# Kernel optimization log

Hardware: AMD Instinct MI355X
Metric: run time of the kernel (lower is better)

The kernel has to match this reference:

```python
import jax, jax.numpy as jnp
import numpy as np

B, S, E, H = 2, 2048, 1024, 16
D = E // H  # head_dim = 64

def setup_inputs() -> dict:
    key = jax.random.key(0)
    ks = jax.random.split(key, 9)
    scale = 1.0 / np.sqrt(E)
    inp = {"x": jax.random.normal(ks[0], (B, S, E), dtype=jnp.float32)}
    for i, name in enumerate(["q", "k", "v", "o"]):
        inp[f"W{name}"] = jax.random.uniform(ks[1 + 2 * i], (E, E), jnp.float32, -scale, scale)
        inp[f"b{name}"] = jax.random.uniform(ks[2 + 2 * i], (E,), jnp.float32, -scale, scale)
    return inp

def reference(x, Wq, bq, Wk, bk, Wv, bv, Wo, bo):
    b, s, e = x.shape
    q = x @ Wq + bq
    k = x @ Wk + bk
    v = x @ Wv + bv
    # Faithful to source: view(B, H, S, D) with NO transpose -> splits the
    # sequence dimension across heads (each head sees a contiguous chunk of
    # s*d elements reinterpreted as [s, d]).
    q = q.reshape(b, H, s, D)
    k = k.reshape(b, H, s, D)
    v = v.reshape(b, H, s, D)
    scores = jnp.einsum("bhqd,bhkd->bhqk", q, k) / np.sqrt(D)
    # mask=False in source still adds a zeros mask (no-op); omitted.
    probs = jax.nn.softmax(scores, axis=-1)
    xhat = jnp.einsum("bhqk,bhkd->bhqd", probs, v)
    # transpose(1, 2).contiguous().view(B, S, E)
    xhat = xhat.transpose(0, 2, 1, 3).reshape(b, s, e)
    return xhat @ Wo + bo
```

## Files before the change

kernel.cpp:

```cpp
#include <hip/hip_runtime.h>
#include <hip/hip_bf16.h>
#include <math.h>

#define B_ 2
#define S_ 2048
#define E_ 1024
#define H_ 16
#define D_ 64

typedef __attribute__((ext_vector_type(8))) short short8;
typedef __attribute__((ext_vector_type(4))) float f32x4;
typedef __attribute__((ext_vector_type(4))) unsigned short us4;
typedef __attribute__((ext_vector_type(8))) unsigned short us8;
typedef unsigned short ushort_t;

#define MFMA16 __builtin_amdgcn_mfma_f32_16x16x32_bf16

__device__ __forceinline__ ushort_t f2bf(float f) {
    unsigned int u = __float_as_uint(f);
    u += 0x7FFFu + ((u >> 16) & 1u);
    return (ushort_t)(u >> 16);
}
__device__ __forceinline__ float bf2f(ushort_t h) {
    return __uint_as_float((unsigned int)h << 16);
}
__device__ __forceinline__ ushort_t f2bf_fast(float f) {
    __hip_bfloat16 h = __float2bfloat16(f);
    return *reinterpret_cast<ushort_t*>(&h);
}

__device__ __forceinline__ void gload16(const void* g, void* l) {
    __builtin_amdgcn_global_load_lds(
        (__attribute__((address_space(1))) void*)(unsigned long long)g,
        (__attribute__((address_space(3))) void*)(unsigned int)(unsigned long long)l,
        16, 0, 0);
}

__global__ __launch_bounds__(256)
void split_x(const float* __restrict__ in, ushort_t* __restrict__ hi)
{
    const size_t base = ((size_t)blockIdx.x * 256 + threadIdx.x) * 8;
    float v[8];
    *reinterpret_cast<float4*>(&v[0]) = *reinterpret_cast<const float4*>(&in[base]);
    *reinterpret_cast<float4*>(&v[4]) = *reinterpret_cast<const float4*>(&in[base + 4]);
    us8 h;
#pragma unroll
    for (int j = 0; j < 8; ++j) h[j] = f2bf(v[j]);
    *reinterpret_cast<us8*>(&hi[base]) = h;
}

__global__ __launch_bounds__(256)
void wsplit_t(const float* __restrict__ Wq, const float* __restrict__ Wk,
              const float* __restrict__ Wv, const float* __restrict__ Wo,
              ushort_t* __restrict__ Wth, ushort_t* __restrict__ Wtl)
{
    __shared__ float T[64][65];
    const int tid = threadIdx.x;
    const int z = blockIdx.z;
    const float* W = (z == 0) ? Wq : (z == 1) ? Wk : (z == 2) ? Wv : Wo;
    const int kt = blockIdx.y * 64;
    const int nt = blockIdx.x * 64;

    const int lr = (tid >> 4) * 4;
    const int lc = (tid & 15) * 4;
#pragma unroll
    for (int i = 0; i < 4; ++i) {
        float4 v = *reinterpret_cast<const float4*>(&W[(size_t)(kt + lr + i) * 1024 + nt + lc]);
        T[lr + i][lc + 0] = v.x; T[lr + i][lc + 1] = v.y;
        T[lr + i][lc + 2] = v.z; T[lr + i][lc + 3] = v.w;
    }
    __syncthreads();

    const int n = tid >> 2;
    const int kc = (tid & 3) * 16;
    us8 h[2], l[2];
#pragma unroll
    for (int u = 0; u < 2; ++u)
#pragma unroll
        for (int j = 0; j < 8; ++j) {
            float v = T[kc + u * 8 + j][n];
            ushort_t hh = f2bf(v);
            h[u][j] = hh;
            l[u][j] = f2bf(v - bf2f(hh));
        }
    ushort_t* dh = Wth + ((size_t)z * 1024 + nt + n) * 1024 + kt + kc;
    ushort_t* dl = Wtl + ((size_t)z * 1024 + nt + n) * 1024 + kt + kc;
    *reinterpret_cast<us8*>(dh)     = h[0];
    *reinterpret_cast<us8*>(dh + 8) = h[1];
    *reinterpret_cast<us8*>(dl)     = l[0];
    *reinterpret_cast<us8*>(dl + 8) = l[1];
}

__global__ __launch_bounds__(256, 3)
void gemm_qkv(const ushort_t* __restrict__ xh, const ushort_t* __restrict__ Wth,
              const float* __restrict__ bq, const float* __restrict__ bk,
              const float* __restrict__ bv,
              ushort_t* __restrict__ Qb, ushort_t* __restrict__ Kb,
              ushort_t* __restrict__ Vb, float qalpha)
{
    __shared__ ushort_t As[128 * 32], Bs[128 * 32];
    const int which = blockIdx.x >> 3;
    const int n0 = (blockIdx.x & 7) * 128;
    const int m0 = blockIdx.y * 128;
    const ushort_t* Bh = Wth + (size_t)which * 1024 * 1024;
    const float* bias = (which == 0) ? bq : (which == 1) ? bk : bv;
    ushort_t* out = (which == 0) ? Qb : (which == 1) ? Kb : Vb;
    const float alpha = (which == 0) ? qalpha : 1.0f;

    const int tid  = threadIdx.x;
    const int lane = tid & 63;
    const int w    = tid >> 6;
    const int l15  = lane & 15;
    const int g    = lane >> 4;
    const int wr   = w >> 1;
    const int wc   = w & 1;

    const int sr  = lane >> 2;
    const int scz = (lane & 3) ^ ((sr >> 1) & 3);
    const int sc  = scz * 8;
    const int j0 = w * 2, j1 = j0 + 1;

    const ushort_t* gA0 = xh + (size_t)(m0 + j0 * 16 + sr) * 1024 + sc;
    const ushort_t* gA1 = xh + (size_t)(m0 + j1 * 16 + sr) * 1024 + sc;
    const ushort_t* gB0 = Bh + (size_t)(n0 + j0 * 16 + sr) * 1024 + sc;
    const ushort_t* gB1 = Bh + (size_t)(n0 + j1 * 16 + sr) * 1024 + sc;

    const int sx  = (l15 >> 1) & 3;
    const int rd1 = (((g >> 1) + 0) ^ sx) * 8 + (g & 1) * 4;
    const int rd2 = (((g >> 1) + 2) ^ sx) * 8 + (g & 1) * 4;

    f32x4 acc[4][4];
#pragma unroll
    for (int i = 0; i < 4; ++i)
#pragma unroll
        for (int j = 0; j < 4; ++j) { acc[i][j][0] = 0.f; acc[i][j][1] = 0.f; acc[i][j][2] = 0.f; acc[i][j][3] = 0.f; }

    for (int kt = 0; kt < 32; ++kt) {
        const int k0 = kt * 32;
        if (kt) __syncthreads();
        gload16(gA0 + k0, As + j0 * 512);
        gload16(gA1 + k0, As + j1 * 512);
        gload16(gB0 + k0, Bs + j0 * 512);
        gload16(gB1 + k0, Bs + j1 * 512);
        asm volatile("s_waitcnt vmcnt(0)" ::: "memory");
        __syncthreads();

        short8 bh[4];
#pragma unroll
        for (int nb = 0; nb < 4; ++nb) {
            const int rb = (wc * 64 + nb * 16 + l15) * 32;
            union { us4 h[2]; short8 s; } u;
            u.h[0] = *reinterpret_cast<const us4*>(Bs + rb + rd1);
            u.h[1] = *reinterpret_cast<const us4*>(Bs + rb + rd2);
            bh[nb] = u.s;
        }
#pragma unroll
        for (int mb = 0; mb < 4; ++mb) {
            const int rb = (wr * 64 + mb * 16 + l15) * 32;
            union { us4 h[2]; short8 s; } ua;
            ua.h[0] = *reinterpret_cast<const us4*>(As + rb + rd1);
            ua.h[1] = *reinterpret_cast<const us4*>(As + rb + rd2);
            const short8 ah = ua.s;
#pragma unroll
            for (int nb = 0; nb < 4; ++nb)
                acc[mb][nb] = MFMA16(ah, bh[nb], acc[mb][nb], 0, 0, 0);
        }
    }

    float bvv[4];
#pragma unroll
    for (int nb = 0; nb < 4; ++nb) bvv[nb] = bias[n0 + wc * 64 + nb * 16 + l15];
#pragma unroll
    for (int mb = 0; mb < 4; ++mb)
#pragma unroll
        for (int r = 0; r < 4; ++r) {
            const size_t row = m0 + wr * 64 + mb * 16 + 4 * g + r;
#pragma unroll
            for (int nb = 0; nb < 4; ++nb) {
                const float vv = (acc[mb][nb][r] + bvv[nb]) * alpha;
                out[row * 1024 + n0 + wc * 64 + nb * 16 + l15] = f2bf(vv);
            }
        }
}

__global__ __launch_bounds__(256, 2)
void gemm_o64(const ushort_t* __restrict__ Ah, const ushort_t* __restrict__ Al,
              const ushort_t* __restrict__ Bh, const ushort_t* __restrict__ Bl,
              const float* __restrict__ bias, float* __restrict__ out)
{
    __shared__ ushort_t AsH[128 * 32], AsL[128 * 32], BsH[64 * 32], BsL[64 * 32];
    const int tid  = threadIdx.x;
    const int lane = tid & 63;
    const int w    = tid >> 6;
    const int l15  = lane & 15;
    const int g    = lane >> 4;
    const int wr   = w >> 1;
    const int wc   = w & 1;
    const int n0 = blockIdx.x * 64;
    const int m0 = blockIdx.y * 128;

    const int sr  = lane >> 2;
    const int scz = (lane & 3) ^ ((sr >> 1) & 3);
    const int sc  = scz * 8;
    const int ja0 = 2 * w, ja1 = 2 * w + 1;

    const ushort_t* gAh0 = Ah + (size_t)(m0 + ja0 * 16 + sr) * 1024 + sc;
    const ushort_t* gAh1 = Ah + (size_t)(m0 + ja1 * 16 + sr) * 1024 + sc;
    const ushort_t* gAl0 = Al + (size_t)(m0 + ja0 * 16 + sr) * 1024 + sc;
    const ushort_t* gAl1 = Al + (size_t)(m0 + ja1 * 16 + sr) * 1024 + sc;
    const ushort_t* gBh0 = Bh + (size_t)(n0 + w * 16 + sr) * 1024 + sc;
    const ushort_t* gBl0 = Bl + (size_t)(n0 + w * 16 + sr) * 1024 + sc;

    const int sx  = (l15 >> 1) & 3;
    const int rd1 = (((g >> 1) + 0) ^ sx) * 8 + (g & 1) * 4;
    const int rd2 = (((g >> 1) + 2) ^ sx) * 8 + (g & 1) * 4;

    f32x4 acc[4][2];
#pragma unroll
    for (int i = 0; i < 4; ++i)
#pragma unroll
        for (int j = 0; j < 2; ++j) { acc[i][j][0] = 0.f; acc[i][j][1] = 0.f; acc[i][j][2] = 0.f; acc[i][j][3] = 0.f; }

    for (int kt = 0; kt < 32; ++kt) {
        const int k0 = kt * 32;
        if (kt) __syncthreads();
        gload16(gAh0 + k0, AsH + ja0 * 512);
        gload16(gAh1 + k0, AsH + ja1 * 512);
        gload16(gAl0 + k0, AsL + ja0 * 512);
        gload16(gAl1 + k0, AsL + ja1 * 512);
        gload16(gBh0 + k0, BsH + w * 512);
        gload16(gBl0 + k0, BsL + w * 512);
        asm volatile("s_waitcnt vmcnt(0)" ::: "memory");
        __syncthreads();

        short8 bh[2], bl[2];
#pragma unroll
        for (int nb = 0; nb < 2; ++nb) {
            const int rb = (wc * 32 + nb * 16 + l15) * 32;
            union { us4 h[2]; short8 s; } u;
            u.h[0] = *reinterpret_cast<const us4*>(BsH + rb + rd1);
            u.h[1] = *reinterpret_cast<const us4*>(BsH + rb + rd2);
            bh[nb] = u.s;
            union { us4 h[2]; short8 s; } v;
            v.h[0] = *reinterpret_cast<const us4*>(BsL + rb + rd1);
            v.h[1] = *reinterpret_cast<const us4*>(BsL + rb + rd2);
            bl[nb] = v.s;
        }
#pragma unroll
        for (int mb = 0; mb < 4; ++mb) {
            const int rb = (wr * 64 + mb * 16 + l15) * 32;
            union { us4 h[2]; short8 s; } ua;
            ua.h[0] = *reinterpret_cast<const us4*>(AsH + rb + rd1);
            ua.h[1] = *reinterpret_cast<const us4*>(AsH + rb + rd2);
            union { us4 h[2]; short8 s; } ul;
            ul.h[0] = *reinterpret_cast<const us4*>(AsL + rb + rd1);
            ul.h[1] = *reinterpret_cast<const us4*>(AsL + rb + rd2);
            const short8 ah = ua.s, al = ul.s;
#pragma unroll
            for (int nb = 0; nb < 2; ++nb) {
                acc[mb][nb] = MFMA16(ah, bh[nb], acc[mb][nb], 0, 0, 0);
                acc[mb][nb] = MFMA16(al, bh[nb], acc[mb][nb], 0, 0, 0);
                acc[mb][nb] = MFMA16(ah, bl[nb], acc[mb][nb], 0, 0, 0);
            }
        }
    }

    float bvv[2];
#pragma unroll
    for (int nb = 0; nb < 2; ++nb) bvv[nb] = bias[n0 + wc * 32 + nb * 16 + l15];
#pragma unroll
    for (int mb = 0; mb < 4; ++mb)
#pragma unroll
        for (int r = 0; r < 4; ++r) {
            const size_t row = m0 + wr * 64 + mb * 16 + 4 * g + r;
#pragma unroll
            for (int nb = 0; nb < 2; ++nb)
                out[row * 1024 + n0 + wc * 32 + nb * 16 + l15] = acc[mb][nb][r] + bvv[nb];
        }
}

__global__ __launch_bounds__(256, 2)
void attn_mfma(const ushort_t* __restrict__ Q, const ushort_t* __restrict__ K,
               const ushort_t* __restrict__ V, ushort_t* __restrict__ XHh,
               ushort_t* __restrict__ XHl)
{
    __shared__ __align__(16) ushort_t Kf[4 * 2 * 64 * 8];
    __shared__ __align__(16) ushort_t Vf[4 * 2 * 64 * 8];

    const int tid  = threadIdx.x;
    const int w    = tid >> 6;
    const int lane = tid & 63;
    const int l15  = lane & 15;
    const int g    = lane >> 4;

    const int L  = blockIdx.x;
    const int qb = (L >> 3) & 15;
    const int bh = (L & 7) | ((L >> 7) << 3);
    const int b  = bh >> 4;
    const int hh = bh & 15;
    const size_t hoff = (size_t)b * S_ * E_ + (size_t)hh * S_ * D_;
    const ushort_t* Qh = Q + hoff;
    const ushort_t* Kh = K + hoff;
    const ushort_t* Vh = V + hoff;

    const int qw = qb * 128 + w * 32;

    short8 qf[2][2];
#pragma unroll
    for (int qg = 0; qg < 2; ++qg)
#pragma unroll
        for (int m = 0; m < 2; ++m) {
            const ushort_t* src = &Qh[(size_t)(qw + 16 * qg + l15) * D_ + 32 * m + 4 * g];
            us4 lo = *reinterpret_cast<const us4*>(src);
            us4 hi = *reinterpret_cast<const us4*>(src + 16);
            union { us4 h[2]; short8 s; } u;
            u.h[0] = lo; u.h[1] = hi;
            qf[qg][m] = u.s;
        }

    const int kr  = tid >> 2;
    const int kc0 = tid & 3;
    const int kkc = tid >> 4;
    const int vdc = tid & 15;
    const int vmc = kkc >> 3;
    const int vh  = (kkc >> 2) & 1;
    const int vg  = kkc & 3;
    const int vn  = vdc >> 2;

    f32x4 o[2][4];
#pragma unroll
    for (int qg = 0; qg < 2; ++qg)
#pragma unroll
        for (int n = 0; n < 4; ++n)
#pragma unroll
            for (int r = 0; r < 4; ++r) o[qg][n][r] = 0.f;

    float mrun[2] = {-1e30f, -1e30f};
    float lrun[2] = {0.f, 0.f};

    us8 kreg[2];
    us4 vreg[4];
#pragma unroll
    for (int u = 0; u < 2; ++u)
        kreg[u] = *reinterpret_cast<const us8*>(&Kh[(size_t)kr * D_ + 8 * (kc0 + 4 * u)]);
#pragma unroll
    for (int i = 0; i < 4; ++i)
        vreg[i] = *reinterpret_cast<const us4*>(&Vh[(size_t)(4 * kkc + i) * D_ + 4 * vdc]);

    for (int kt = 0; kt < S_ / 64; ++kt) {
        __syncthreads();

#pragma unroll
        for (int u = 0; u < 2; ++u) {
            const int c8 = kc0 + 4 * u;
            const int m = c8 >> 2;
            const int h = (c8 >> 1) & 1;
#pragma unroll
            for (int jh = 0; jh < 2; ++jh) {
                const int gk = (2 * c8 + jh) & 3;
                const int slot = gk * 16 + (kr & 15);
                us4 val;
#pragma unroll
                for (int i = 0; i < 4; ++i) val[i] = (ushort_t)kreg[u][4 * jh + i];
                *reinterpret_cast<us4*>(&Kf[((((kr >> 4) * 2 + m) * 64 + slot) * 8) + h * 4]) = val;
            }
        }
#pragma unroll
        for (int jj = 0; jj < 4; ++jj) {
            us4 val;
#pragma unroll
            for (int i = 0; i < 4; ++i) val[i] = vreg[i][jj];
            const int pos  = 4 * (vdc & 3) + jj;
            const int posx = pos ^ vg ^ (vn << 2);
            const int slot = vg * 16 + posx;
            *reinterpret_cast<us4*>(&Vf[(((vn * 2 + vmc) * 64 + slot) * 8) + vh * 4]) = val;
        }
        __syncthreads();

        if (kt + 1 < S_ / 64) {
            const int nt = kt + 1;
#pragma unroll
            for (int u = 0; u < 2; ++u)
                kreg[u] = *reinterpret_cast<const us8*>(&Kh[(size_t)(nt * 64 + kr) * D_ + 8 * (kc0 + 4 * u)]);
#pragma unroll
            for (int i = 0; i < 4; ++i)
                vreg[i] = *reinterpret_cast<const us4*>(&Vh[(size_t)(nt * 64 + 4 * kkc + i) * D_ + 4 * vdc]);
        }

        short8 kf[4][2];
#pragma unroll
        for (int kkb = 0; kkb < 4; ++kkb)
#pragma unroll
            for (int m = 0; m < 2; ++m)
                kf[kkb][m] = *reinterpret_cast<const short8*>(&Kf[((kkb * 2 + m) * 64 + lane) * 8]);

        f32x4 s[2][4];
#pragma unroll
        for (int qg = 0; qg < 2; ++qg)
#pragma unroll
            for (int kkb = 0; kkb < 4; ++kkb) {
                f32x4 z; z[0] = 0.f; z[1] = 0.f; z[2] = 0.f; z[3] = 0.f;
                z = MFMA16(kf[kkb][0], qf[qg][0], z, 0, 0, 0);
                s[qg][kkb] = MFMA16(kf[kkb][1], qf[qg][1], z, 0, 0, 0);
            }

        short8 vf[4][2];
#pragma unroll
        for (int n = 0; n < 4; ++n)
#pragma unroll
            for (int m = 0; m < 2; ++m) {
                const int posr = (lane & 15) ^ (lane >> 4) ^ (n << 2);
                const int slot = (lane & 48) | posr;
                vf[n][m] = *reinterpret_cast<const short8*>(&Vf[((n * 2 + m) * 64 + slot) * 8]);
            }

#pragma unroll
        for (int qg = 0; qg < 2; ++qg) {
            float t = s[qg][0][0];
#pragma unroll
            for (int kkb = 0; kkb < 4; ++kkb)
#pragma unroll
                for (int r = 0; r < 4; ++r) t = fmaxf(t, s[qg][kkb][r]);
            t = fmaxf(t, __shfl_xor(t, 16));
            t = fmaxf(t, __shfl_xor(t, 32));
            const float mnew = fmaxf(mrun[qg], t);
            const float corr = __builtin_amdgcn_exp2f(mrun[qg] - mnew);

            float rs = 0.f;
#pragma unroll
            for (int kkb = 0; kkb < 4; ++kkb)
#pragma unroll
                for (int r = 0; r < 4; ++r) {
                    const float p = __builtin_amdgcn_exp2f(s[qg][kkb][r] - mnew);
                    s[qg][kkb][r] = p;
                    rs += p;
                }
            rs += __shfl_xor(rs, 16);
            rs += __shfl_xor(rs, 32);
            lrun[qg] = lrun[qg] * corr + rs;
            mrun[qg] = mnew;

#pragma unroll
            for (int r = 0; r < 4; ++r) {
                const float c4 = __shfl(corr, 4 * g + r);
#pragma unroll
                for (int n = 0; n < 4; ++n) o[qg][n][r] *= c4;
            }

            short8 pa[2];
#pragma unroll
            for (int m = 0; m < 2; ++m) {
                us8 tmp;
#pragma unroll
                for (int r = 0; r < 4; ++r) {
                    tmp[r]     = f2bf_fast(s[qg][2 * m][r]);
                    tmp[r + 4] = f2bf_fast(s[qg][2 * m + 1][r]);
                }
                union { us8 u8; short8 s8; } cvt; cvt.u8 = tmp;
                pa[m] = cvt.s8;
            }
#pragma unroll
            for (int n = 0; n < 4; ++n) {
                o[qg][n] = MFMA16(pa[0], vf[n][0], o[qg][n], 0, 0, 0);
                o[qg][n] = MFMA16(pa[1], vf[n][1], o[qg][n], 0, 0, 0);
            }
        }
    }

#pragma unroll
    for (int qg = 0; qg < 2; ++qg) {
        const float invl = 1.f / lrun[qg];
#pragma unroll
        for (int r = 0; r < 4; ++r) {
            const float iv = __shfl(invl, 4 * g + r);
            const int row = qw + 16 * qg + 4 * g + r;
            const size_t base = ((size_t)b * S_ + row) * E_ + hh * D_ + l15;
#pragma unroll
            for (int n = 0; n < 4; ++n) {
                const float vv = o[qg][n][r] * iv;
                const ushort_t hi = f2bf(vv);
                XHh[base + 16 * n] = hi;
                XHl[base + 16 * n] = f2bf(vv - bf2f(hi));
            }
        }
    }
}

extern "C" void kernel_launch(void* const* d_in, const int* in_sizes, int n_in,
                              void* d_out, int out_size, void* d_ws, size_t ws_size,
                              hipStream_t stream) {
    (void)in_sizes; (void)n_in; (void)out_size; (void)ws_size;
    const float* x  = (const float*)d_in[0];
    const float* Wq = (const float*)d_in[1];
    const float* bq = (const float*)d_in[2];
    const float* Wk = (const float*)d_in[3];
    const float* bk = (const float*)d_in[4];
    const float* Wv = (const float*)d_in[5];
    const float* bv = (const float*)d_in[6];
    const float* Wo = (const float*)d_in[7];
    const float* bo = (const float*)d_in[8];
    float* out = (float*)d_out;

    char* ws = (char*)d_ws;
    const size_t MB8 = 8ull * 1024 * 1024;
    ushort_t* xhi = (ushort_t*)(ws);
    ushort_t* XHl = (ushort_t*)(ws + MB8);
    ushort_t* Wth = (ushort_t*)(ws + 2 * MB8);
    ushort_t* Wtl = (ushort_t*)(ws + 3 * MB8);
    ushort_t* Qb  = (ushort_t*)(ws + 4 * MB8);
    ushort_t* Kb  = (ushort_t*)(ws + 5 * MB8);
    ushort_t* Vb  = (ushort_t*)(ws + 6 * MB8);
    ushort_t* XHh = xhi;

    const float qalpha = 0.125f * 1.4426950408889634f;

    split_x<<<dim3(2048), dim3(256), 0, stream>>>(x, xhi);
    wsplit_t<<<dim3(16, 16, 4), dim3(256), 0, stream>>>(Wq, Wk, Wv, Wo, Wth, Wtl);

    gemm_qkv<<<dim3(24, 32), dim3(256), 0, stream>>>(xhi, Wth,
                                                     bq, bk, bv, Qb, Kb, Vb, qalpha);

    attn_mfma<<<dim3(512), dim3(256), 0, stream>>>(Qb, Kb, Vb, XHh, XHl);

    gemm_o64<<<dim3(16, 32), dim3(256), 0, stream>>>(XHh, XHl,
                                                     Wth + 3ull * 1024 * 1024,
                                                     Wtl + 3ull * 1024 * 1024,
                                                     bo, out);
}
```

Baseline: 159.5 us.

## Process 128-key tiles per iteration in attention, halving barriers and softmax rescales

The attention loop now handles 128 keys per iteration (two 64-key LDS halves) instead of 64. This halves the number of __syncthreads pairs and online-softmax max/corr/rescale steps per key. It drops the register prefetch of the next tile, so global loads are issued at the top of each iteration and waited on before the LDS stores. The larger score array also raises register pressure, which risks spills or lower occupancy under launch_bounds(256,2).

```diff
diff --git a/kernel.cpp b/kernel.cpp
--- a/kernel.cpp
+++ b/kernel.cpp
@@ -284,8 +284,8 @@
                const ushort_t* __restrict__ V, ushort_t* __restrict__ XHh,
                ushort_t* __restrict__ XHl)
 {
-    __shared__ __align__(16) ushort_t Kf[4 * 2 * 64 * 8];
-    __shared__ __align__(16) ushort_t Vf[4 * 2 * 64 * 8];
+    __shared__ __align__(16) ushort_t Kf[2][4 * 2 * 64 * 8];
+    __shared__ __align__(16) ushort_t Vf[2][4 * 2 * 64 * 8];
 
     const int tid  = threadIdx.x;
     const int w    = tid >> 6;
@@ -338,89 +338,78 @@
     float mrun[2] = {-1e30f, -1e30f};
     float lrun[2] = {0.f, 0.f};
 
-    us8 kreg[2];
-    us4 vreg[4];
-#pragma unroll
-    for (int u = 0; u < 2; ++u)
-        kreg[u] = *reinterpret_cast<const us8*>(&Kh[(size_t)kr * D_ + 8 * (kc0 + 4 * u)]);
-#pragma unroll
-    for (int i = 0; i < 4; ++i)
-        vreg[i] = *reinterpret_cast<const us4*>(&Vh[(size_t)(4 * kkc + i) * D_ + 4 * vdc]);
-
-    for (int kt = 0; kt < S_ / 64; ++kt) {
+    for (int kt = 0; kt < S_ / 128; ++kt) {
+        us8 kreg[2][2];
+        us4 vreg[2][4];
+#pragma unroll
+        for (int hf = 0; hf < 2; ++hf) {
+            const int rowb = kt * 128 + hf * 64;
+#pragma unroll
+            for (int u = 0; u < 2; ++u)
+                kreg[hf][u] = *reinterpret_cast<const us8*>(&Kh[(size_t)(rowb + kr) * D_ + 8 * (kc0 + 4 * u)]);
+#pragma unroll
+            for (int i = 0; i < 4; ++i)
+                vreg[hf][i] = *reinterpret_cast<const us4*>(&Vh[(size_t)(rowb + 4 * kkc + i) * D_ + 4 * vdc]);
+        }
+
         __syncthreads();
 
 #pragma unroll
-        for (int u = 0; u < 2; ++u) {
-            const int c8 = kc0 + 4 * u;
-            const int m = c8 >> 2;
-            const int h = (c8 >> 1) & 1;
-#pragma unroll
-            for (int jh = 0; jh < 2; ++jh) {
-                const int gk = (2 * c8 + jh) & 3;
-                const int slot = gk * 16 + (kr & 15);
+        for (int hf = 0; hf < 2; ++hf) {
+#pragma unroll
+            for (int u = 0; u < 2; ++u) {
+                const int c8 = kc0 + 4 * u;
+                const int m = c8 >> 2;
+                const int h = (c8 >> 1) & 1;
+#pragma unroll
+                for (int jh = 0; jh < 2; ++jh) {
+                    const int gk = (2 * c8 + jh) & 3;
+                    const int slot = gk * 16 + (kr & 15);
+                    us4 val;
+#pragma unroll
+                    for (int i = 0; i < 4; ++i) val[i] = (ushort_t)kreg[hf][u][4 * jh + i];
+                    *reinterpret_cast<us4*>(&Kf[hf][((((kr >> 4) * 2 + m) * 64 + slot) * 8) + h * 4]) = val;
+                }
+            }
+#pragma unroll
+            for (int jj = 0; jj < 4; ++jj) {
                 us4 val;
 #pragma unroll
-                for (int i = 0; i < 4; ++i) val[i] = (ushort_t)kreg[u][4 * jh + i];
-                *reinterpret_cast<us4*>(&Kf[((((kr >> 4) * 2 + m) * 64 + slot) * 8) + h * 4]) = val;
-            }
-        }
-#pragma unroll
-        for (int jj = 0; jj < 4; ++jj) {
-            us4 val;
-#pragma unroll
-            for (int i = 0; i < 4; ++i) val[i] = vreg[i][jj];
-            const int pos  = 4 * (vdc & 3) + jj;
-            const int posx = pos ^ vg ^ (vn << 2);
-            const int slot = vg * 16 + posx;
-            *reinterpret_cast<us4*>(&Vf[(((vn * 2 + vmc) * 64 + slot) * 8) + vh * 4]) = val;
+                for (int i = 0; i < 4; ++i) val[i] = vreg[hf][i][jj];
+                const int pos  = 4 * (vdc & 3) + jj;
+                const int posx = pos ^ vg ^ (vn << 2);
+                const int slot = vg * 16 + posx;
+                *reinterpret_cast<us4*>(&Vf[hf][(((vn * 2 + vmc) * 64 + slot) * 8) + vh * 4]) = val;
+            }
         }
         __syncthreads();
 
-        if (kt + 1 < S_ / 64) {
-            const int nt = kt + 1;
-#pragma unroll
-            for (int u = 0; u < 2; ++u)
-                kreg[u] = *reinterpret_cast<const us8*>(&Kh[(size_t)(nt * 64 + kr) * D_ + 8 * (kc0 + 4 * u)]);
-#pragma unroll
-            for (int i = 0; i < 4; ++i)
-                vreg[i] = *reinterpret_cast<const us4*>(&Vh[(size_t)(nt * 64 + 4 * kkc + i) * D_ + 4 * vdc]);
-        }
-
-        short8 kf[4][2];
-#pragma unroll
-        for (int kkb = 0; kkb < 4; ++kkb)
-#pragma unroll
-            for (int m = 0; m < 2; ++m)
-                kf[kkb][m] = *reinterpret_cast<const short8*>(&Kf[((kkb * 2 + m) * 64 + lane) * 8]);
-
-        f32x4 s[2][4];
-#pragma unroll
-        for (int qg = 0; qg < 2; ++qg)
-#pragma unroll
-            for (int kkb = 0; kkb < 4; ++kkb) {
-                f32x4 z; z[0] = 0.f; z[1] = 0.f; z[2] = 0.f; z[3] = 0.f;
-                z = MFMA16(kf[kkb][0], qf[qg][0], z, 0, 0, 0);
-                s[qg][kkb] = MFMA16(kf[kkb][1], qf[qg][1], z, 0, 0, 0);
-            }
-
-        short8 vf[4][2];
-#pragma unroll
-        for (int n = 0; n < 4; ++n)
-#pragma unroll
-            for (int m = 0; m < 2; ++m) {
-                const int posr = (lane & 15) ^ (lane >> 4) ^ (n << 2);
-                const int slot = (lane & 48) | posr;
-                vf[n][m] = *reinterpret_cast<const short8*>(&Vf[((n * 2 + m) * 64 + slot) * 8]);
-            }
+        f32x4 s[2][8];
+#pragma unroll
+        for (int hf = 0; hf < 2; ++hf) {
+            short8 kf[4][2];
+#pragma unroll
+            for (int kkb = 0; kkb < 4; ++kkb)
+#pragma unroll
+                for (int m = 0; m < 2; ++m)
+                    kf[kkb][m] = *reinterpret_cast<const short8*>(&Kf[hf][((kkb * 2 + m) * 64 + lane) * 8]);
+#pragma unroll
+            for (int qg = 0; qg < 2; ++qg)
+#pragma unroll
+                for (int kkb = 0; kkb < 4; ++kkb) {
+                    f32x4 z; z[0] = 0.f; z[1] = 0.f; z[2] = 0.f; z[3] = 0.f;
+                    z = MFMA16(kf[kkb][0], qf[qg][0], z, 0, 0, 0);
+                    s[qg][hf * 4 + kkb] = MFMA16(kf[kkb][1], qf[qg][1], z, 0, 0, 0);
+                }
+        }
 
 #pragma unroll
         for (int qg = 0; qg < 2; ++qg) {
             float t = s[qg][0][0];
 #pragma unroll
-            for (int kkb = 0; kkb < 4; ++kkb)
-#pragma unroll
-                for (int r = 0; r < 4; ++r) t = fmaxf(t, s[qg][kkb][r]);
+            for (int j = 0; j < 8; ++j)
+#pragma unroll
+                for (int r = 0; r < 4; ++r) t = fmaxf(t, s[qg][j][r]);
             t = fmaxf(t, __shfl_xor(t, 16));
             t = fmaxf(t, __shfl_xor(t, 32));
             const float mnew = fmaxf(mrun[qg], t);
@@ -428,11 +417,11 @@
 
             float rs = 0.f;
 #pragma unroll
-            for (int kkb = 0; kkb < 4; ++kkb)
+            for (int j = 0; j < 8; ++j)
 #pragma unroll
                 for (int r = 0; r < 4; ++r) {
-                    const float p = __builtin_amdgcn_exp2f(s[qg][kkb][r] - mnew);
-                    s[qg][kkb][r] = p;
+                    const float p = __builtin_amdgcn_exp2f(s[qg][j][r] - mnew);
+                    s[qg][j][r] = p;
                     rs += p;
                 }
             rs += __shfl_xor(rs, 16);
@@ -446,23 +435,38 @@
 #pragma unroll
                 for (int n = 0; n < 4; ++n) o[qg][n][r] *= c4;
             }
-
-            short8 pa[2];
-#pragma unroll
-            for (int m = 0; m < 2; ++m) {
-                us8 tmp;
-#pragma unroll
-                for (int r = 0; r < 4; ++r) {
-                    tmp[r]     = f2bf_fast(s[qg][2 * m][r]);
-                    tmp[r + 4] = f2bf_fast(s[qg][2 * m + 1][r]);
+        }
+
+#pragma unroll
+        for (int hf = 0; hf < 2; ++hf) {
+            short8 vf[4][2];
+#pragma unroll
+            for (int n = 0; n < 4; ++n)
+#pragma unroll
+                for (int m = 0; m < 2; ++m) {
+                    const int posr = (lane & 15) ^ (lane >> 4) ^ (n << 2);
+                    const int slot = (lane & 48) | posr;
+                    vf[n][m] = *reinterpret_cast<const short8*>(&Vf[hf][((n * 2 + m) * 64 + slot) * 8]);
                 }
-                union { us8 u8; short8 s8; } cvt; cvt.u8 = tmp;
-                pa[m] = cvt.s8;
-            }
-#pragma unroll
-            for (int n = 0; n < 4; ++n) {
-                o[qg][n] = MFMA16(pa[0], vf[n][0], o[qg][n], 0, 0, 0);
-                o[qg][n] = MFMA16(pa[1], vf[n][1], o[qg][n], 0, 0, 0);
+#pragma unroll
+            for (int qg = 0; qg < 2; ++qg) {
+                short8 pa[2];
+#pragma unroll
+                for (int m = 0; m < 2; ++m) {
+                    us8 tmp;
+#pragma unroll
+                    for (int r = 0; r < 4; ++r) {
+                        tmp[r]     = f2bf_fast(s[qg][hf * 4 + 2 * m][r]);
+                        tmp[r + 4] = f2bf_fast(s[qg][hf * 4 + 2 * m + 1][r]);
+                    }
+                    union { us8 u8; short8 s8; } cvt; cvt.u8 = tmp;
+                    pa[m] = cvt.s8;
+                }
+#pragma unroll
+                for (int n = 0; n < 4; ++n) {
+                    o[qg][n] = MFMA16(pa[0], vf[n][0], o[qg][n], 0, 0, 0);
+                    o[qg][n] = MFMA16(pa[1], vf[n][1], o[qg][n], 0, 0, 0);
+                }
             }
         }
     }
```

Result: faster. 150.7 us (-5.5%).

## Split attention KV range across two wave groups and merge softmax partials

Applied to the files above, without the earlier changes.

The attention kernel now launches 512 threads per block: two groups of four waves each handle half of the key/value sequence with separate shared-memory tiles. At the end, group 1 writes its partial outputs and running max/sum to LDS, and group 0 merges them flash-decoding style before storing. The aim is more parallelism and occupancy per query tile, trading away the register prefetch of the next K/V tile. It also adds an LDS merge step and tighter register limits from launch_bounds(512,4).

```diff
diff --git a/kernel.cpp b/kernel.cpp
--- a/kernel.cpp
+++ b/kernel.cpp
@@ -279,17 +279,20 @@
         }
 }
 
-__global__ __launch_bounds__(256, 2)
+__global__ __launch_bounds__(512, 4)
 void attn_mfma(const ushort_t* __restrict__ Q, const ushort_t* __restrict__ K,
                const ushort_t* __restrict__ V, ushort_t* __restrict__ XHh,
                ushort_t* __restrict__ XHl)
 {
-    __shared__ __align__(16) ushort_t Kf[4 * 2 * 64 * 8];
-    __shared__ __align__(16) ushort_t Vf[4 * 2 * 64 * 8];
+    __shared__ __align__(16) ushort_t SM[4][4096];
+    __shared__ float ML[4][2][16][2];
 
     const int tid  = threadIdx.x;
-    const int w    = tid >> 6;
+    const int w8   = tid >> 6;
+    const int grp  = w8 >> 2;
+    const int wl   = w8 & 3;
     const int lane = tid & 63;
+    const int ltid = tid & 255;
     const int l15  = lane & 15;
     const int g    = lane >> 4;
 
@@ -303,7 +306,7 @@
     const ushort_t* Kh = K + hoff;
     const ushort_t* Vh = V + hoff;
 
-    const int qw = qb * 128 + w * 32;
+    const int qw = qb * 128 + wl * 32;
 
     short8 qf[2][2];
 #pragma unroll
@@ -318,15 +321,18 @@
             qf[qg][m] = u.s;
         }
 
-    const int kr  = tid >> 2;
-    const int kc0 = tid & 3;
-    const int kkc = tid >> 4;
-    const int vdc = tid & 15;
+    const int kr  = ltid >> 2;
+    const int kc0 = ltid & 3;
+    const int kkc = ltid >> 4;
+    const int vdc = ltid & 15;
     const int vmc = kkc >> 3;
     const int vh  = (kkc >> 2) & 1;
     const int vg  = kkc & 3;
     const int vn  = vdc >> 2;
 
+    ushort_t* KfG = SM[grp];
+    ushort_t* VfG = SM[2 + grp];
+
     f32x4 o[2][4];
 #pragma unroll
     for (int qg = 0; qg < 2; ++qg)
@@ -338,16 +344,17 @@
     float mrun[2] = {-1e30f, -1e30f};
     float lrun[2] = {0.f, 0.f};
 
-    us8 kreg[2];
-    us4 vreg[4];
-#pragma unroll
-    for (int u = 0; u < 2; ++u)
-        kreg[u] = *reinterpret_cast<const us8*>(&Kh[(size_t)kr * D_ + 8 * (kc0 + 4 * u)]);
-#pragma unroll
-    for (int i = 0; i < 4; ++i)
-        vreg[i] = *reinterpret_cast<const us4*>(&Vh[(size_t)(4 * kkc + i) * D_ + 4 * vdc]);
-
-    for (int kt = 0; kt < S_ / 64; ++kt) {
+    for (int kt = 0; kt < 16; ++kt) {
+        const int rowb = grp * 1024 + kt * 64;
+        us8 kreg[2];
+#pragma unroll
+        for (int u = 0; u < 2; ++u)
+            kreg[u] = *reinterpret_cast<const us8*>(&Kh[(size_t)(rowb + kr) * D_ + 8 * (kc0 + 4 * u)]);
+        us4 vreg[4];
+#pragma unroll
+        for (int i = 0; i < 4; ++i)
+            vreg[i] = *reinterpret_cast<const us4*>(&Vh[(size_t)(rowb + 4 * kkc + i) * D_ + 4 * vdc]);
+
         __syncthreads();
 
 #pragma unroll
@@ -362,7 +369,7 @@
                 us4 val;
 #pragma unroll
                 for (int i = 0; i < 4; ++i) val[i] = (ushort_t)kreg[u][4 * jh + i];
-                *reinterpret_cast<us4*>(&Kf[((((kr >> 4) * 2 + m) * 64 + slot) * 8) + h * 4]) = val;
+                *reinterpret_cast<us4*>(&KfG[((((kr >> 4) * 2 + m) * 64 + slot) * 8) + h * 4]) = val;
             }
         }
 #pragma unroll
@@ -373,26 +380,16 @@
             const int pos  = 4 * (vdc & 3) + jj;
             const int posx = pos ^ vg ^ (vn << 2);
             const int slot = vg * 16 + posx;
-            *reinterpret_cast<us4*>(&Vf[(((vn * 2 + vmc) * 64 + slot) * 8) + vh * 4]) = val;
+            *reinterpret_cast<us4*>(&VfG[(((vn * 2 + vmc) * 64 + slot) * 8) + vh * 4]) = val;
         }
         __syncthreads();
 
-        if (kt + 1 < S_ / 64) {
-            const int nt = kt + 1;
-#pragma unroll
-            for (int u = 0; u < 2; ++u)
-                kreg[u] = *reinterpret_cast<const us8*>(&Kh[(size_t)(nt * 64 + kr) * D_ + 8 * (kc0 + 4 * u)]);
-#pragma unroll
-            for (int i = 0; i < 4; ++i)
-                vreg[i] = *reinterpret_cast<const us4*>(&Vh[(size_t)(nt * 64 + 4 * kkc + i) * D_ + 4 * vdc]);
-        }
-
         short8 kf[4][2];
 #pragma unroll
         for (int kkb = 0; kkb < 4; ++kkb)
 #pragma unroll
             for (int m = 0; m < 2; ++m)
-                kf[kkb][m] = *reinterpret_cast<const short8*>(&Kf[((kkb * 2 + m) * 64 + lane) * 8]);
+                kf[kkb][m] = *reinterpret_cast<const short8*>(&KfG[((kkb * 2 + m) * 64 + lane) * 8]);
 
         f32x4 s[2][4];
 #pragma unroll
@@ -411,7 +408,7 @@
             for (int m = 0; m < 2; ++m) {
                 const int posr = (lane & 15) ^ (lane >> 4) ^ (n << 2);
                 const int slot = (lane & 48) | posr;
-                vf[n][m] = *reinterpret_cast<const short8*>(&Vf[((n * 2 + m) * 64 + slot) * 8]);
+                vf[n][m] = *reinterpret_cast<const short8*>(&VfG[((n * 2 + m) * 64 + slot) * 8]);
             }
 
 #pragma unroll
@@ -467,20 +464,47 @@
         }
     }
 
-#pragma unroll
-    for (int qg = 0; qg < 2; ++qg) {
-        const float invl = 1.f / lrun[qg];
-#pragma unroll
-        for (int r = 0; r < 4; ++r) {
-            const float iv = __shfl(invl, 4 * g + r);
-            const int row = qw + 16 * qg + 4 * g + r;
-            const size_t base = ((size_t)b * S_ + row) * E_ + hh * D_ + l15;
-#pragma unroll
-            for (int n = 0; n < 4; ++n) {
-                const float vv = o[qg][n][r] * iv;
-                const ushort_t hi = f2bf(vv);
-                XHh[base + 16 * n] = hi;
-                XHl[base + 16 * n] = f2bf(vv - bf2f(hi));
+    __syncthreads();
+    float* OX = reinterpret_cast<float*>(&SM[0][0]);
+    if (grp == 1) {
+#pragma unroll
+        for (int qg = 0; qg < 2; ++qg) {
+#pragma unroll
+            for (int n = 0; n < 4; ++n)
+#pragma unroll
+                for (int r = 0; r < 4; ++r)
+                    OX[(((wl * 64 + lane) * 2 + qg) * 16) + n * 4 + r] = o[qg][n][r];
+            if (lane < 16) {
+                ML[wl][qg][lane][0] = mrun[qg];
+                ML[wl][qg][lane][1] = lrun[qg];
+            }
+        }
+    }
+    __syncthreads();
+    if (grp == 0) {
+#pragma unroll
+        for (int qg = 0; qg < 2; ++qg) {
+            const float m1 = ML[wl][qg][l15][0];
+            const float l1 = ML[wl][qg][l15][1];
+            const float mm = fmaxf(mrun[qg], m1);
+            const float c0 = __builtin_amdgcn_exp2f(mrun[qg] - mm);
+            const float c1 = __builtin_amdgcn_exp2f(m1 - mm);
+            const float invl = 1.f / (lrun[qg] * c0 + l1 * c1);
+#pragma unroll
+            for (int r = 0; r < 4; ++r) {
+                const float c0r = __shfl(c0, 4 * g + r);
+                const float c1r = __shfl(c1, 4 * g + r);
+                const float iv  = __shfl(invl, 4 * g + r);
+                const int row = qw + 16 * qg + 4 * g + r;
+                const size_t base = ((size_t)b * S_ + row) * E_ + hh * D_ + l15;
+#pragma unroll
+                for (int n = 0; n < 4; ++n) {
+                    const float o1 = OX[(((wl * 64 + lane) * 2 + qg) * 16) + n * 4 + r];
+                    const float vv = (o[qg][n][r] * c0r + o1 * c1r) * iv;
+                    const ushort_t hi = f2bf(vv);
+                    XHh[base + 16 * n] = hi;
+                    XHl[base + 16 * n] = f2bf(vv - bf2f(hi));
+                }
             }
         }
     }
@@ -520,7 +544,7 @@
     gemm_qkv<<<dim3(24, 32), dim3(256), 0, stream>>>(xhi, Wth,
                                                      bq, bk, bv, Qb, Kb, Vb, qalpha);
 
-    attn_mfma<<<dim3(512), dim3(256), 0, stream>>>(Qb, Kb, Vb, XHh, XHl);
+    attn_mfma<<<dim3(512), dim3(512), 0, stream>>>(Qb, Kb, Vb, XHh, XHl);
 
     gemm_o64<<<dim3(16, 32), dim3(256), 0, stream>>>(XHh, XHl,
                                                      Wth + 3ull * 1024 * 1024,
```

Result: slower. 168.5 us (+5.6%).
